# Optimization experiments

Hardware: AMD Instinct MI355X
Metric: run time of the kernel (lower is better)

Reference implementation:

```python
import jax, jax.numpy as jnp
import numpy as np

N, C, H, W = 8, 19, 512, 512
BORDER_DILATE = 5
BORDER_POWER = 0.5
BORDER_WEIGHT = 1.0
IGNORE = 255


def setup_inputs() -> dict:
    key = jax.random.key(0)
    k1, k2 = jax.random.split(key)
    slices = jax.random.normal(k1, (N, C, H, W), dtype=jnp.float32)
    targets = jax.random.randint(k2, (N, 1, H, W), 0, C).astype(jnp.int64)
    return {"slices": slices, "targets": targets}


def class_boundaries(m):
    # m: bool (N, K, H, W); XOR of vertical/horizontal neighbors, padded like torch
    tb = m[:, :, 1:, :] ^ m[:, :, :-1, :]          # pad bottom row with 0
    lr = m[:, :, :, 1:] ^ m[:, :, :, :-1]          # pad leftmost column with 0
    tb = jnp.pad(tb, ((0, 0), (0, 0), (0, 1), (0, 0)))
    lr = jnp.pad(lr, ((0, 0), (0, 0), (0, 0), (1, 0)))
    return tb | lr


def _min_scan_axis(d, axis):
    # forward then backward chamfer pass d[i] = min(d[i], d[i -/+ 1] + 1) along `axis`
    x = jnp.moveaxis(d, axis, 0)

    def step(carry, row):
        new = jnp.minimum(row, carry + 1.0)
        return new, new

    _, fwd = jax.lax.scan(step, x[0], x[1:])
    x = jnp.concatenate([x[:1], fwd], axis=0)
    _, bwd = jax.lax.scan(step, x[-1], x[:-1][::-1])
    x = jnp.concatenate([bwd[::-1], x[-1:]], axis=0)
    return jnp.moveaxis(x, 0, axis)


def distance_matrix(border):
    # border: bool (N, K, H, W). Penalty matches torch.tensor((N,1,H,W)).sum()
    penalty = jnp.float32(N + 1 + H + W)
    d = jnp.where(border, 0.0, penalty)
    d = _min_scan_axis(d, 2)   # H forward + backward
    d = _min_scan_axis(d, 3)   # W forward + backward
    return jax.nn.relu(d - jnp.float32(BORDER_DILATE))


def _forward(slices, targets):
    t = targets[:, 0]  # (N, H, W)
    # cross-entropy, reduction='sum', ignore_index
    logp = jax.nn.log_softmax(slices, axis=1)
    valid = t != IGNORE
    t_safe = jnp.where(valid, t, 0)
    picked = jnp.take_along_axis(logp, t_safe[:, None], axis=1)[:, 0]  # (N,H,W)
    ce = -jnp.sum(jnp.where(valid, picked, 0.0))

    # border loss: vectorized over all class ids (torch loops over unique targets)
    sm = jax.nn.softmax(slices, axis=1)                      # (N,C,H,W)
    pred = jnp.argmax(slices, axis=1, keepdims=True)         # (N,1,H,W)
    cls = jnp.arange(C)[None, :, None, None]
    pred_oh = pred == cls                                    # (N,C,H,W) bool
    tgt_oh = targets == cls                                  # (N,C,H,W) bool
    pred_b = class_boundaries(pred_oh).astype(sm.dtype)
    tgt_d = distance_matrix(class_boundaries(tgt_oh))
    present = jnp.any(tgt_oh, axis=(0, 2, 3)).astype(sm.dtype)  # only ids in targets
    border = jnp.sum(sm * pred_b * tgt_d * present[None, :, None, None])

    return ce + jnp.float32(BORDER_WEIGHT) * border ** jnp.float32(BORDER_POWER)


def reference(slices, targets):
    return _forward(slices, targets)
```

## Files before the change

kernel.cpp:

```cpp
#include <hip/hip_runtime.h>

#define NN 8
#define CC 19
#define HH 512
#define WW 512
#define HW (HH*WW)
#define NPIX (NN*HW)
#define NPLANE (NN*CC)
#define BIGV (1<<20)
#define M7 0x7F7F7F7Fu

__device__ unsigned char g_tT[NPIX];
__device__ unsigned char g_pred[NPIX];
__device__ float g_lse[NPIX];
__device__ unsigned char g_inter[(size_t)NPLANE*HW];
__device__ float g_ce;
__device__ float g_part[64][16];
__device__ unsigned int g_present_mask;

__device__ __forceinline__ unsigned int eqz(unsigned int x) {
  unsigned int y = (x & M7) + M7;
  return ~(y | x | M7);
}

__global__ __launch_bounds__(256) void k_pixel(const float* __restrict__ slices,
                                               const int* __restrict__ targets) {
  int bp = blockIdx.x * 2048;
  int n = bp >> 18;
  int r = bp & (HW - 1);
  int wv = threadIdx.x >> 6;
  int lane = threadIdx.x & 63;
  int o0 = wv * 512 + lane * 4;
  int o1 = o0 + 256;
  const float* base = slices + (size_t)n * CC * HW + r;

  const int4* t4p = (const int4*)(targets + bp);
  int4 ta = t4p[o0 >> 2];
  int4 tb = t4p[o1 >> 2];
  int t[8] = {ta.x, ta.y, ta.z, ta.w, tb.x, tb.y, tb.z, tb.w};

  float m[8], s[8], pk[8];
  int a[8];
  {
    float4 x0 = *(const float4*)(base + o0);
    float4 x1 = *(const float4*)(base + o1);
    float x[8] = {x0.x, x0.y, x0.z, x0.w, x1.x, x1.y, x1.z, x1.w};
#pragma unroll
    for (int j = 0; j < 8; ++j) {
      m[j] = x[j];
      a[j] = 0;
      s[j] = __expf(x[j]);
      pk[j] = (t[j] == 0) ? x[j] : 0.f;
    }
  }
#pragma unroll 2
  for (int c = 1; c < CC; ++c) {
    float4 x0 = *(const float4*)(base + (size_t)c * HW + o0);
    float4 x1 = *(const float4*)(base + (size_t)c * HW + o1);
    float x[8] = {x0.x, x0.y, x0.z, x0.w, x1.x, x1.y, x1.z, x1.w};
#pragma unroll
    for (int j = 0; j < 8; ++j) {
      if (x[j] > m[j]) { m[j] = x[j]; a[j] = c; }
      s[j] += __expf(x[j]);
      pk[j] = (c == t[j]) ? x[j] : pk[j];
    }
  }

  float l[8];
  float ce_local = 0.f;
  unsigned int msk = 0u;
#pragma unroll
  for (int j = 0; j < 8; ++j) {
    l[j] = __logf(s[j]);
    if (t[j] != 255) ce_local += l[j] - pk[j];
    if ((unsigned)t[j] < CC) msk |= 1u << t[j];
  }

  ((float4*)(g_lse + bp))[o0 >> 2] = make_float4(l[0], l[1], l[2], l[3]);
  ((float4*)(g_lse + bp))[o1 >> 2] = make_float4(l[4], l[5], l[6], l[7]);
  ((uchar4*)(g_pred + bp))[o0 >> 2] =
      make_uchar4((unsigned char)a[0], (unsigned char)a[1],
                  (unsigned char)a[2], (unsigned char)a[3]);
  ((uchar4*)(g_pred + bp))[o1 >> 2] =
      make_uchar4((unsigned char)a[4], (unsigned char)a[5],
                  (unsigned char)a[6], (unsigned char)a[7]);
#pragma unroll
  for (int j = 0; j < 8; ++j) {
    int p = bp + ((j < 4) ? (o0 + j) : (o1 + j - 4));
    int h = (p >> 9) & 511;
    int w = p & 511;
    g_tT[((size_t)n << 18) + (size_t)w * HH + h] = (unsigned char)t[j];
  }

  __shared__ float sred[256];
  __shared__ unsigned int smsk[256];
  sred[threadIdx.x] = ce_local;
  smsk[threadIdx.x] = msk;
  __syncthreads();
  for (int st = 128; st > 0; st >>= 1) {
    if (threadIdx.x < st) {
      sred[threadIdx.x] += sred[threadIdx.x + st];
      smsk[threadIdx.x] |= smsk[threadIdx.x + st];
    }
    __syncthreads();
  }
  if (threadIdx.x == 0) {
    atomicAdd(&g_ce, sred[0]);
    atomicOr(&g_present_mask, smsk[0]);
  }
}

__global__ __launch_bounds__(512, 4) void k_hscan() {
  int plane = blockIdx.x >> 3;
  int wt = blockIdx.x & 7;
  int hc = threadIdx.x >> 6;
  int wl = threadIdx.x & 63;
  int c = plane % CC;
  int n = plane / CC;
  int w = wt * 64 + wl;
  const unsigned char* colC = g_tT + ((size_t)n << 18) + (size_t)w * HH + hc * 64;

  uint4 ca = *(const uint4*)(colC);
  uint4 cb = *(const uint4*)(colC + 16);
  uint4 cc2 = *(const uint4*)(colC + 32);
  uint4 cd = *(const uint4*)(colC + 48);
  unsigned int cw[16];
  cw[0]=ca.x; cw[1]=ca.y; cw[2]=ca.z; cw[3]=ca.w;
  cw[4]=cb.x; cw[5]=cb.y; cw[6]=cb.z; cw[7]=cb.w;
  cw[8]=cc2.x; cw[9]=cc2.y; cw[10]=cc2.z; cw[11]=cc2.w;
  cw[12]=cd.x; cw[13]=cd.y; cw[14]=cd.z; cw[15]=cd.w;

  unsigned int lw[16];
#pragma unroll
  for (int i = 0; i < 16; ++i) lw[i] = __shfl_up(cw[i], 1, 64);
  if (wl == 0) {
    if (w > 0) {
      const unsigned char* colL = colC - HH;
      uint4 la = *(const uint4*)(colL);
      uint4 lb = *(const uint4*)(colL + 16);
      uint4 lc = *(const uint4*)(colL + 32);
      uint4 ld = *(const uint4*)(colL + 48);
      lw[0]=la.x; lw[1]=la.y; lw[2]=la.z; lw[3]=la.w;
      lw[4]=lb.x; lw[5]=lb.y; lw[6]=lb.z; lw[7]=lb.w;
      lw[8]=lc.x; lw[9]=lc.y; lw[10]=lc.z; lw[11]=lc.w;
      lw[12]=ld.x; lw[13]=ld.y; lw[14]=ld.z; lw[15]=ld.w;
    } else {
#pragma unroll
      for (int i = 0; i < 16; ++i) lw[i] = cw[i];
    }
  }

  __shared__ unsigned char s_edge[8][64];
  s_edge[hc][wl] = (unsigned char)(cw[0] & 255u);
  __syncthreads();
  unsigned int tnl = (hc < 7) ? (unsigned int)s_edge[hc + 1][wl]
                              : ((cw[15] >> 24) & 255u);

  unsigned int bc = (unsigned int)c * 0x01010101u;
  int v[64];
  int prev = BIGV;
#pragma unroll
  for (int i = 0; i < 16; ++i) {
    unsigned int cwi = cw[i];
    unsigned int nxt = (i < 15) ? (cw[i + 1] & 255u) : tnl;
    unsigned int tnw = (cwi >> 8) | (nxt << 24);
    unsigned int zc = eqz(cwi ^ bc);
    unsigned int zn = eqz(tnw ^ bc);
    unsigned int zl = eqz(lw[i] ^ bc);
    unsigned int bb = (zc ^ zn) | (zc ^ zl);
#pragma unroll
    for (int k = 0; k < 4; ++k) {
      int bit = (int)((bb >> (8 * k + 7)) & 1u);
      prev = min(bit ? 0 : 255, prev + 1);
      v[4 * i + k] = prev;
    }
  }

  __shared__ int s_car[8][64];
  s_car[hc][wl] = v[63];
  __syncthreads();
  int F = BIGV;
#pragma unroll
  for (int i = 0; i < 7; ++i)
    if (i < hc) F = min(s_car[i][wl] + 1, F + 64);
#pragma unroll
  for (int k = 0; k < 64; ++k) v[k] = min(v[k], F + k);

#pragma unroll
  for (int k = 62; k >= 0; --k) v[k] = min(v[k], v[k + 1] + 1);

  __syncthreads();
  s_car[hc][wl] = v[0];
  __syncthreads();
  int B = BIGV;
#pragma unroll
  for (int j = 7; j >= 1; --j)
    if (j > hc) B = min(s_car[j][wl] + 1, B + 64);

  unsigned char* outb = g_inter + (((size_t)plane * 8 + wt) * HH + hc * 64) * 64 + wl;
#pragma unroll
  for (int k = 0; k < 64; ++k) {
    int outv = min(v[k], B + (63 - k));
    outb[(size_t)k * 64] = (unsigned char)outv;
  }
}

__global__ __launch_bounds__(512) void k_wscan(const float* __restrict__ slices) {
  int plane = blockIdx.x >> 6;
  int hg = blockIdx.x & 63;
  int wv = threadIdx.x >> 6;
  int lane = threadIdx.x & 63;
  int h = hg * 8 + wv;
  int c = plane % CC;
  int n = plane / CC;

  const unsigned char* rowp =
      g_inter + (((size_t)plane * 8 + (lane >> 3)) * HH + h) * 64 + (lane & 7) * 8;
  uint2 r8 = *(const uint2*)rowp;

  int d0[8];
#pragma unroll
  for (int k = 0; k < 4; ++k) {
    d0[k]     = (int)((r8.x >> (k * 8)) & 255u);
    d0[k + 4] = (int)((r8.y >> (k * 8)) & 255u);
  }
  int ls[8];
  ls[0] = d0[0];
#pragma unroll
  for (int k = 1; k < 8; ++k) ls[k] = min(d0[k], ls[k - 1] + 1);
  int u = ls[7] - 8 * lane;
#pragma unroll
  for (int o = 1; o < 64; o <<= 1) {
    int t = __shfl_up(u, o, 64);
    if (lane >= o) u = min(u, t);
  }
  int cf = __shfl_up(u, 1, 64);
  int carry = (lane == 0) ? BIGV : cf + 8 * (lane - 1);
  int f[8];
#pragma unroll
  for (int k = 0; k < 8; ++k) f[k] = min(ls[k], carry + k + 1);
  int bs[8];
  bs[7] = f[7];
#pragma unroll
  for (int k = 6; k >= 0; --k) bs[k] = min(f[k], bs[k + 1] + 1);
  int mm = bs[0] + 8 * lane;
#pragma unroll
  for (int o = 1; o < 64; o <<= 1) {
    int t = __shfl_down(mm, o, 64);
    if (lane + o < 64) mm = min(mm, t);
  }
  int mb = __shfl_down(mm, 1, 64);
  int carryb = (lane == 63) ? BIGV : mb - 8 * lane;

  float acc = 0.f;
#pragma unroll
  for (int k = 0; k < 8; ++k) {
    int D = min(bs[k], carryb - k);
    int d = D - 5;
    if (d > 0) {
      int w = lane * 8 + k;
      int pix = (n * HH + h) * WW + w;
      int pcv = g_pred[pix];
      int pnv = (h + 1 < HH) ? g_pred[pix + WW] : pcv;
      int plv = (w > 0) ? g_pred[pix - 1] : pcv;
      bool ec = (pcv == c);
      if ((ec != (pnv == c)) || (ec != (plv == c))) {
        float x = slices[((size_t)n * CC + c) * HW + (size_t)h * WW + w];
        float smv = __expf(x - g_lse[pix]);
        acc += smv * (float)d;
      }
    }
  }

#pragma unroll
  for (int o = 32; o > 0; o >>= 1) acc += __shfl_down(acc, o, 64);
  if (lane == 0) {
    float pres = (g_present_mask >> c) & 1u ? 1.f : 0.f;
    atomicAdd(&g_part[blockIdx.x & 63][0], acc * pres);
  }
}

__global__ void k_final(float* __restrict__ out) {
  int t = threadIdx.x;
  float b = g_part[t][0];
#pragma unroll
  for (int o = 32; o > 0; o >>= 1) b += __shfl_down(b, o, 64);
  if (t == 0) {
    out[0] = g_ce + sqrtf(b);
    g_ce = 0.f;
    g_present_mask = 0u;
  }
  g_part[t][0] = 0.f;
}

extern "C" void kernel_launch(void* const* d_in, const int* in_sizes, int n_in,
                              void* d_out, int out_size, void* d_ws, size_t ws_size,
                              hipStream_t stream) {
  const float* slices = (const float*)d_in[0];
  const int* targets = (const int*)d_in[1];
  float* out = (float*)d_out;
  (void)d_ws; (void)ws_size; (void)in_sizes; (void)n_in; (void)out_size;

  hipLaunchKernelGGL(k_pixel, dim3(NPIX / 2048), dim3(256), 0, stream, slices, targets);
  hipLaunchKernelGGL(k_hscan, dim3(NPLANE * 8), dim3(512), 0, stream);
  hipLaunchKernelGGL(k_wscan, dim3(NPLANE * 64), dim3(512), 0, stream, slices);
  hipLaunchKernelGGL(k_final, dim3(1), dim3(64), 0, stream, out);
}
```

Baseline: 130.1 us.

## Stage intermediate tiles in shared memory for W-scan and fuse final reduction

k_wscan now handles a 64-row band per block. It loads the tiled intermediate distance bytes for that band with coalesced uint2 reads into a 32KB shared tile, then each wave scans 8 rows from shared memory instead of doing strided 8-byte global reads. The separate k_final launch is removed: a last-block-done counter lets the final block reduce the partial sums and write the output. This cuts launch overhead and improves read coalescing, but the grid is 8x smaller, so there is less parallelism and each wave has more serial work.

Result: slower. 151.0 us (+16.1%).

```diff
diff --git a/kernel.cpp b/kernel.cpp
--- a/kernel.cpp
+++ b/kernel.cpp
@@ -17,6 +17,7 @@
 __device__ float g_ce;
 __device__ float g_part[64][16];
 __device__ unsigned int g_present_mask;
+__device__ unsigned int g_done;
 
 __device__ __forceinline__ unsigned int eqz(unsigned int x) {
   unsigned int y = (x & M7) + M7;
@@ -205,92 +206,117 @@
   }
 }
 
-__global__ __launch_bounds__(512) void k_wscan(const float* __restrict__ slices) {
-  int plane = blockIdx.x >> 6;
-  int hg = blockIdx.x & 63;
+__global__ __launch_bounds__(512, 4) void k_wscan(const float* __restrict__ slices,
+                                                  float* __restrict__ out) {
+  int plane = blockIdx.x >> 3;
+  int hcb = blockIdx.x & 7;
   int wv = threadIdx.x >> 6;
   int lane = threadIdx.x & 63;
-  int h = hg * 8 + wv;
   int c = plane % CC;
   int n = plane / CC;
-
-  const unsigned char* rowp =
-      g_inter + (((size_t)plane * 8 + (lane >> 3)) * HH + h) * 64 + (lane & 7) * 8;
-  uint2 r8 = *(const uint2*)rowp;
-
-  int d0[8];
-#pragma unroll
-  for (int k = 0; k < 4; ++k) {
-    d0[k]     = (int)((r8.x >> (k * 8)) & 255u);
-    d0[k + 4] = (int)((r8.y >> (k * 8)) & 255u);
-  }
-  int ls[8];
-  ls[0] = d0[0];
-#pragma unroll
-  for (int k = 1; k < 8; ++k) ls[k] = min(d0[k], ls[k - 1] + 1);
-  int u = ls[7] - 8 * lane;
-#pragma unroll
-  for (int o = 1; o < 64; o <<= 1) {
-    int t = __shfl_up(u, o, 64);
-    if (lane >= o) u = min(u, t);
-  }
-  int cf = __shfl_up(u, 1, 64);
-  int carry = (lane == 0) ? BIGV : cf + 8 * (lane - 1);
-  int f[8];
-#pragma unroll
-  for (int k = 0; k < 8; ++k) f[k] = min(ls[k], carry + k + 1);
-  int bs[8];
-  bs[7] = f[7];
-#pragma unroll
-  for (int k = 6; k >= 0; --k) bs[k] = min(f[k], bs[k + 1] + 1);
-  int mm = bs[0] + 8 * lane;
-#pragma unroll
-  for (int o = 1; o < 64; o <<= 1) {
-    int t = __shfl_down(mm, o, 64);
-    if (lane + o < 64) mm = min(mm, t);
-  }
-  int mb = __shfl_down(mm, 1, 64);
-  int carryb = (lane == 63) ? BIGV : mb - 8 * lane;
-
+  size_t pibase = (size_t)plane * HW;
+
+  __shared__ unsigned char s_tile[64 * 512];
+  __shared__ int s_last;
+
+#pragma unroll
+  for (int wt = 0; wt < 8; ++wt) {
+    const uint2* src = (const uint2*)(g_inter + pibase + (size_t)wt * 32768 + (size_t)hcb * 4096);
+    uint2 d = src[threadIdx.x];
+    int g = threadIdx.x * 8;
+    int hl = g >> 6;
+    int w8 = g & 63;
+    *(uint2*)&s_tile[hl * 512 + wt * 64 + w8] = d;
+  }
+  __syncthreads();
+
+  unsigned int pmask = g_present_mask;
+  float pres = ((pmask >> c) & 1u) ? 1.f : 0.f;
   float acc = 0.f;
-#pragma unroll
-  for (int k = 0; k < 8; ++k) {
-    int D = min(bs[k], carryb - k);
-    int d = D - 5;
-    if (d > 0) {
-      int w = lane * 8 + k;
-      int pix = (n * HH + h) * WW + w;
-      int pcv = g_pred[pix];
-      int pnv = (h + 1 < HH) ? g_pred[pix + WW] : pcv;
-      int plv = (w > 0) ? g_pred[pix - 1] : pcv;
-      bool ec = (pcv == c);
-      if ((ec != (pnv == c)) || (ec != (plv == c))) {
-        float x = slices[((size_t)n * CC + c) * HW + (size_t)h * WW + w];
-        float smv = __expf(x - g_lse[pix]);
-        acc += smv * (float)d;
+
+  for (int k2 = 0; k2 < 8; ++k2) {
+    int hl = wv * 8 + k2;
+    int h = hcb * 64 + hl;
+    uint2 r8 = *(const uint2*)&s_tile[hl * 512 + lane * 8];
+
+    int d0[8];
+#pragma unroll
+    for (int k = 0; k < 4; ++k) {
+      d0[k]     = (int)((r8.x >> (k * 8)) & 255u);
+      d0[k + 4] = (int)((r8.y >> (k * 8)) & 255u);
+    }
+    int ls[8];
+    ls[0] = d0[0];
+#pragma unroll
+    for (int k = 1; k < 8; ++k) ls[k] = min(d0[k], ls[k - 1] + 1);
+    int u = ls[7] - 8 * lane;
+#pragma unroll
+    for (int o = 1; o < 64; o <<= 1) {
+      int t = __shfl_up(u, o, 64);
+      if (lane >= o) u = min(u, t);
+    }
+    int cf = __shfl_up(u, 1, 64);
+    int carry = (lane == 0) ? BIGV : cf + 8 * (lane - 1);
+    int f[8];
+#pragma unroll
+    for (int k = 0; k < 8; ++k) f[k] = min(ls[k], carry + k + 1);
+    int bs[8];
+    bs[7] = f[7];
+#pragma unroll
+    for (int k = 6; k >= 0; --k) bs[k] = min(f[k], bs[k + 1] + 1);
+    int mm = bs[0] + 8 * lane;
+#pragma unroll
+    for (int o = 1; o < 64; o <<= 1) {
+      int t = __shfl_down(mm, o, 64);
+      if (lane + o < 64) mm = min(mm, t);
+    }
+    int mb = __shfl_down(mm, 1, 64);
+    int carryb = (lane == 63) ? BIGV : mb - 8 * lane;
+
+#pragma unroll
+    for (int k = 0; k < 8; ++k) {
+      int D = min(bs[k], carryb - k);
+      int d = D - 5;
+      if (d > 0) {
+        int w = lane * 8 + k;
+        int pix = (n * HH + h) * WW + w;
+        int pcv = g_pred[pix];
+        int pnv = (h + 1 < HH) ? g_pred[pix + WW] : pcv;
+        int plv = (w > 0) ? g_pred[pix - 1] : pcv;
+        bool ec = (pcv == c);
+        if ((ec != (pnv == c)) || (ec != (plv == c))) {
+          float x = slices[((size_t)n * CC + c) * HW + (size_t)h * WW + w];
+          float smv = __expf(x - g_lse[pix]);
+          acc += smv * (float)d;
+        }
       }
     }
   }
 
 #pragma unroll
   for (int o = 32; o > 0; o >>= 1) acc += __shfl_down(acc, o, 64);
-  if (lane == 0) {
-    float pres = (g_present_mask >> c) & 1u ? 1.f : 0.f;
-    atomicAdd(&g_part[blockIdx.x & 63][0], acc * pres);
-  }
-}
-
-__global__ void k_final(float* __restrict__ out) {
-  int t = threadIdx.x;
-  float b = g_part[t][0];
-#pragma unroll
-  for (int o = 32; o > 0; o >>= 1) b += __shfl_down(b, o, 64);
-  if (t == 0) {
-    out[0] = g_ce + sqrtf(b);
-    g_ce = 0.f;
-    g_present_mask = 0u;
-  }
-  g_part[t][0] = 0.f;
+  if (lane == 0) atomicAdd(&g_part[blockIdx.x & 63][0], acc * pres);
+
+  __syncthreads();
+  if (threadIdx.x == 0) {
+    __threadfence();
+    unsigned int old = atomicAdd(&g_done, 1u);
+    s_last = (old == (unsigned int)(gridDim.x - 1)) ? 1 : 0;
+  }
+  __syncthreads();
+  if (s_last && threadIdx.x < 64) {
+    __threadfence();
+    float b = atomicAdd(&g_part[threadIdx.x][0], 0.f);
+#pragma unroll
+    for (int o = 32; o > 0; o >>= 1) b += __shfl_down(b, o, 64);
+    if (threadIdx.x == 0) {
+      out[0] = g_ce + sqrtf(b);
+      g_ce = 0.f;
+      g_present_mask = 0u;
+      g_done = 0u;
+    }
+    g_part[threadIdx.x][0] = 0.f;
+  }
 }
 
 extern "C" void kernel_launch(void* const* d_in, const int* in_sizes, int n_in,
@@ -303,6 +329,5 @@
 
   hipLaunchKernelGGL(k_pixel, dim3(NPIX / 2048), dim3(256), 0, stream, slices, targets);
   hipLaunchKernelGGL(k_hscan, dim3(NPLANE * 8), dim3(512), 0, stream);
-  hipLaunchKernelGGL(k_wscan, dim3(NPLANE * 64), dim3(512), 0, stream, slices);
-  hipLaunchKernelGGL(k_final, dim3(1), dim3(64), 0, stream, out);
-}
+  hipLaunchKernelGGL(k_wscan, dim3(NPLANE * 8), dim3(512), 0, stream, slices, out);
+}
```
